# Optimization experiments

Measured on AMD Instinct MI355X. Metric: run time of the kernel, lower is better.

The kernel has to match this reference:

```python
import jax, jax.numpy as jnp
import numpy as np

H = 1024
N_HEADS = 8
HEAD_DIM = H // N_HEADS
META_DIM = 256
VOCAB = 32000
MIN_W, MAX_W = 0.1, 5.0
LN_EPS = 1e-5


def _ln(x, g, b):
    mu = jnp.mean(x, axis=-1, keepdims=True)
    var = jnp.var(x, axis=-1, keepdims=True)
    return (x - mu) * jax.lax.rsqrt(var + LN_EPS) * g + b


def setup_inputs() -> dict:
    key = jax.random.key(0)
    ks = jax.random.split(key, 16)
    B, S = 4, 2048
    s = 0.02
    return {
        "hidden_states": jax.random.normal(ks[0], (B, S, H), jnp.float32),
        "token_ids": jax.random.randint(ks[1], (B, S), 0, VOCAB, jnp.int32),
        "attention_mask": jnp.ones((B, S), jnp.bool_),
        "pos_embed": jax.random.normal(ks[2], (1, S, H), jnp.float32),
        # torch nn.MultiheadAttention params
        "in_proj_w": jax.random.normal(ks[3], (3 * H, H), jnp.float32) * s,
        "in_proj_b": jnp.zeros((3 * H,), jnp.float32),
        "out_w": jax.random.normal(ks[4], (H, H), jnp.float32) * s,
        "out_b": jnp.zeros((H,), jnp.float32),
        # meta_network params (torch Linear convention: y = x @ W.T + b)
        "w1": jax.random.normal(ks[5], (META_DIM, 2 * H), jnp.float32) * s,
        "b1": jnp.zeros((META_DIM,), jnp.float32),
        "g1": jnp.ones((META_DIM,), jnp.float32),
        "beta1": jnp.zeros((META_DIM,), jnp.float32),
        "w2": jax.random.normal(ks[6], (META_DIM // 2, META_DIM), jnp.float32) * s,
        "b2": jnp.zeros((META_DIM // 2,), jnp.float32),
        "g2": jnp.ones((META_DIM // 2,), jnp.float32),
        "beta2": jnp.zeros((META_DIM // 2,), jnp.float32),
        "w3": jax.random.normal(ks[7], (1, META_DIM // 2), jnp.float32) * s,
        "b3": jnp.zeros((1,), jnp.float32),
        # tensorized ImportanceMemory.get_importance: one scalar per vocab id
        "importance_table": jax.random.uniform(ks[8], (VOCAB,), jnp.float32) * 0.1,
    }


def reference(hidden_states, token_ids, attention_mask, pos_embed,
              in_proj_w, in_proj_b, out_w, out_b,
              w1, b1, g1, beta1, w2, b2, g2, beta2, w3, b3,
              importance_table):
    B, S, _ = hidden_states.shape
    x = hidden_states + pos_embed[:, :S, :]

    # MultiheadAttention (batch_first, eval mode -> no dropout)
    qkv = x @ in_proj_w.T + in_proj_b                      # [B,S,3H]
    q, k, v = jnp.split(qkv, 3, axis=-1)
    q = q.reshape(B, S, N_HEADS, HEAD_DIM)
    k = k.reshape(B, S, N_HEADS, HEAD_DIM)
    v = v.reshape(B, S, N_HEADS, HEAD_DIM)
    scores = jnp.einsum('bqhd,bkhd->bhqk', q, k) / jnp.sqrt(jnp.float32(HEAD_DIM))
    scores = jnp.where(attention_mask[:, None, None, :], scores, jnp.float32(-1e9))
    attn = jax.nn.softmax(scores, axis=-1)
    ctx = jnp.einsum('bhqk,bkhd->bqhd', attn, v).reshape(B, S, H)
    attended = ctx @ out_w.T + out_b

    combined = jnp.concatenate([x, attended], axis=-1)     # [B,S,2H]
    h = jax.nn.relu(_ln(combined @ w1.T + b1, g1, beta1))
    h = jax.nn.relu(_ln(h @ w2.T + b2, g2, beta2))
    base_weights = (h @ w3.T + b3).squeeze(-1)             # [B,S]

    # tensorized per-token importance lookup + clamp (manual_weights empty)
    importance = importance_table[token_ids]               # gather [B,S]
    weight = jnp.clip(base_weights * (1.0 + importance), MIN_W, MAX_W)
    return jnp.where(attention_mask, weight, 0.0)
```

## Files before the change

kernel.cpp:

```cpp
#include <hip/hip_runtime.h>
#include <hip/hip_bf16.h>
#include <math.h>

typedef __bf16 bf16;
typedef bf16 bf16x8 __attribute__((ext_vector_type(8)));
typedef bf16 bf16x4 __attribute__((ext_vector_type(4)));
typedef float f32x4 __attribute__((ext_vector_type(4)));

#define HDIM 1024
#define NHEADS 8
#define HD 128
#define MD1 256
#define MD2 128
#define LNEPS 1e-5f

__device__ __forceinline__ f32x4 mfma16(bf16x8 a, bf16x8 b, f32x4 c) {
  return __builtin_amdgcn_mfma_f32_16x16x32_bf16(a, b, c, 0, 0, 0);
}

__device__ __forceinline__ void gload_lds16(const bf16* g, bf16* l) {
  __builtin_amdgcn_global_load_lds(
      (const __attribute__((address_space(1))) void*)g,
      (__attribute__((address_space(3))) void*)l, 16, 0, 0);
}

__global__ void k_prep(const float* __restrict__ hs, const float* __restrict__ pos,
                       bf16* __restrict__ xbf, int SH, int total) {
  int i = (blockIdx.x * blockDim.x + threadIdx.x) * 4;
  if (i >= total) return;
  float4 a = *(const float4*)(hs + i);
  float4 p = *(const float4*)(pos + (i % SH));
  bf16x4 o;
  o[0] = (bf16)(a.x + p.x);
  o[1] = (bf16)(a.y + p.y);
  o[2] = (bf16)(a.z + p.z);
  o[3] = (bf16)(a.w + p.w);
  *(bf16x4*)(xbf + i) = o;
}

__global__ void k_cvt(const float* __restrict__ in, bf16* __restrict__ out, int n) {
  int i = (blockIdx.x * blockDim.x + threadIdx.x) * 4;
  if (i >= n) return;
  float4 v = *(const float4*)(in + i);
  bf16x4 o;
  o[0] = (bf16)v.x; o[1] = (bf16)v.y; o[2] = (bf16)v.z; o[3] = (bf16)v.w;
  *(bf16x4*)(out + i) = o;
}

template<bool OUT_BF>
__global__ __launch_bounds__(256) void k_gemm128(
    const bf16* __restrict__ A, const bf16* __restrict__ Bw,
    const float* __restrict__ bias, void* __restrict__ out,
    int N, int K) {
  __shared__ bf16 As[128 * 32];
  __shared__ bf16 Bs[128 * 32];
  const int tid = threadIdx.x;
  const int w = tid >> 6, lane = tid & 63;
  const int quad = lane >> 4, l16 = lane & 15;
  const int wm = w & 1, wn = w >> 1;
  const int tm = blockIdx.x * 128, tn = blockIdx.y * 128;

  const int r0 = tid >> 2;
  const int f0 = (r0 ^ (r0 >> 2)) & 3;
  const int f1 = ((r0 + 64) ^ ((r0 + 64) >> 2)) & 3;
  const int c0 = (((tid & 3) ^ f0) * 8);
  const int c1 = (((tid & 3) ^ f1) * 8);
  const bf16* a0 = A + (size_t)(tm + r0) * K + c0;
  const bf16* a1 = A + (size_t)(tm + r0 + 64) * K + c1;
  const bf16* b0 = Bw + (size_t)(tn + r0) * K + c0;
  const bf16* b1 = Bw + (size_t)(tn + r0 + 64) * K + c1;
  bf16* lA = As + (size_t)tid * 8;
  bf16* lB = Bs + (size_t)tid * 8;

  f32x4 acc[4][4] = {};
  for (int k0 = 0; k0 < K; k0 += 32) {
    gload_lds16(a0 + k0, lA);
    gload_lds16(a1 + k0, lA + 2048);
    gload_lds16(b0 + k0, lB);
    gload_lds16(b1 + k0, lB + 2048);
    __syncthreads();
    bf16x8 af[4], bfr[4];
#pragma unroll
    for (int mt = 0; mt < 4; ++mt) {
      const int r = wm * 64 + mt * 16 + l16;
      af[mt] = *(const bf16x8*)&As[r * 32 + ((quad ^ ((r ^ (r >> 2)) & 3)) << 3)];
    }
#pragma unroll
    for (int nt = 0; nt < 4; ++nt) {
      const int r = wn * 64 + nt * 16 + l16;
      bfr[nt] = *(const bf16x8*)&Bs[r * 32 + ((quad ^ ((r ^ (r >> 2)) & 3)) << 3)];
    }
#pragma unroll
    for (int mt = 0; mt < 4; ++mt)
#pragma unroll
      for (int nt = 0; nt < 4; ++nt)
        acc[mt][nt] = mfma16(af[mt], bfr[nt], acc[mt][nt]);
    __syncthreads();
  }

#pragma unroll
  for (int nt = 0; nt < 4; ++nt) {
    const int col = tn + wn * 64 + nt * 16 + l16;
    const float bv = bias ? bias[col] : 0.f;
#pragma unroll
    for (int mt = 0; mt < 4; ++mt) {
#pragma unroll
      for (int i = 0; i < 4; ++i) {
        const int row = tm + wm * 64 + mt * 16 + quad * 4 + i;
        const float v = acc[mt][nt][i] + bv;
        if (OUT_BF) ((bf16*)out)[(size_t)row * N + col] = (bf16)v;
        else        ((float*)out)[(size_t)row * N + col] = v;
      }
    }
  }
}

template<bool OUT_BF>
__global__ __launch_bounds__(256) void k_gemm_bt(
    const bf16* __restrict__ A1, const bf16* __restrict__ A2, int K1, int K2,
    const bf16* __restrict__ Bw, const float* __restrict__ bias,
    void* __restrict__ out, int N) {
  const int K = K1 + K2;
  __shared__ bf16 As[64][40];
  __shared__ bf16 Bs[64][40];
  const int tid = threadIdx.x;
  const int w = tid >> 6, lane = tid & 63;
  const int quad = lane >> 4, l16 = lane & 15;
  const int tm = blockIdx.x * 64, tn = blockIdx.y * 64;
  const int lr = tid >> 2;
  const int lc = (tid & 3) * 8;

  f32x4 acc[4] = {};
  for (int k0 = 0; k0 < K; k0 += 32) {
    const int kg = k0 + lc;
    const bf16* ap = (kg < K1) ? (A1 + (size_t)(tm + lr) * K1 + kg)
                               : (A2 + (size_t)(tm + lr) * K2 + (kg - K1));
    *(bf16x8*)&As[lr][lc] = *(const bf16x8*)ap;
    *(bf16x8*)&Bs[lr][lc] = *(const bf16x8*)(Bw + (size_t)(tn + lr) * K + kg);
    __syncthreads();
    bf16x8 af = *(const bf16x8*)&As[w * 16 + l16][quad * 8];
#pragma unroll
    for (int c = 0; c < 4; ++c) {
      bf16x8 bfrag = *(const bf16x8*)&Bs[c * 16 + l16][quad * 8];
      acc[c] = mfma16(af, bfrag, acc[c]);
    }
    __syncthreads();
  }
#pragma unroll
  for (int c = 0; c < 4; ++c) {
    const int col = tn + c * 16 + l16;
    const float bv = bias ? bias[col] : 0.f;
#pragma unroll
    for (int i = 0; i < 4; ++i) {
      const int row = tm + w * 16 + quad * 4 + i;
      const float v = acc[c][i] + bv;
      if (OUT_BF) ((bf16*)out)[(size_t)row * N + col] = (bf16)v;
      else        ((float*)out)[(size_t)row * N + col] = v;
    }
  }
}

__global__ __launch_bounds__(256) void k_flash(
    const bf16* __restrict__ qkv, const int* __restrict__ mask,
    bf16* __restrict__ ctx, int S) {
  __shared__ bf16 Ks[64][136];
  __shared__ bf16 Vt[128 * 64];
  __shared__ bf16 Ps[4 * 16 * 64];
  __shared__ float biass[64];
  const int tid = threadIdx.x, w = tid >> 6, lane = tid & 63;
  const int quad = lane >> 4, l16 = lane & 15;
  const int bh = blockIdx.y, b = bh / NHEADS, h = bh % NHEADS;
  const int q0 = blockIdx.x * 64 + w * 16;
  const size_t rstride = 3 * HDIM;
  const bf16* Qb = qkv + (size_t)b * S * rstride + h * HD;
  const bf16* Kb = Qb + HDIM;
  const bf16* Vb = Qb + 2 * HDIM;
  const int* mrow = mask + (size_t)b * S;

  bf16x8 qf[4];
#pragma unroll
  for (int s = 0; s < 4; ++s)
    qf[s] = *(const bf16x8*)(Qb + (size_t)(q0 + l16) * rstride + s * 32 + quad * 8);

  float lsum[4] = {0.f, 0.f, 0.f, 0.f};
  f32x4 o[8] = {};
  const float scale2 = 0.08838834764831845f * 1.4426950408889634f;

  const int nchunk = S / 64;
  bf16x8 kreg[4], vreg[4];
  int mreg = (tid < 64) ? mrow[tid] : 0;
#pragma unroll
  for (int it = 0; it < 4; ++it) {
    const int cid = tid + it * 256, row = cid >> 4, d8 = (cid & 15) * 8;
    kreg[it] = *(const bf16x8*)(Kb + (size_t)row * rstride + d8);
    vreg[it] = *(const bf16x8*)(Vb + (size_t)row * rstride + d8);
  }

  for (int c0 = 0; c0 < nchunk; ++c0) {
    __syncthreads();
#pragma unroll
    for (int it = 0; it < 4; ++it) {
      const int cid = tid + it * 256, row = cid >> 4, d8 = (cid & 15) * 8;
      *(bf16x8*)&Ks[row][d8] = kreg[it];
      const int rb = row >> 3, rlo = row & 7;
#pragma unroll
      for (int j = 0; j < 8; ++j) {
        const int d = d8 + j;
        const int blk = rb ^ ((d ^ (d >> 3)) & 7);
        Vt[d * 64 + blk * 8 + rlo] = vreg[it][j];
      }
    }
    if (tid < 64) biass[tid] = mreg ? 0.f : -1e9f;
    __syncthreads();
    const int cn = (c0 + 1 < nchunk) ? c0 + 1 : c0;
    const int key0n = cn * 64;
    if (tid < 64) mreg = mrow[key0n + tid];
#pragma unroll
    for (int it = 0; it < 4; ++it) {
      const int cid = tid + it * 256, row = cid >> 4, d8 = (cid & 15) * 8;
      kreg[it] = *(const bf16x8*)(Kb + (size_t)(key0n + row) * rstride + d8);
      vreg[it] = *(const bf16x8*)(Vb + (size_t)(key0n + row) * rstride + d8);
    }
#pragma unroll
    for (int g = 0; g < 4; ++g) {
      f32x4 s4 = {};
#pragma unroll
      for (int s = 0; s < 4; ++s) {
        bf16x8 kf = *(const bf16x8*)&Ks[g * 16 + l16][s * 32 + quad * 8];
        s4 = mfma16(qf[s], kf, s4);
      }
      const float bias = biass[g * 16 + l16];
      const int kb2 = 2 * g + (l16 >> 3), klo = l16 & 7;
#pragma unroll
      for (int i = 0; i < 4; ++i) {
        const float p = exp2f(fmaf(s4[i], scale2, bias));
        lsum[i] += p;
        const int r = quad * 4 + i;
        Ps[w * 1024 + r * 64 + ((kb2 ^ (r & 7)) << 3) + klo] = (bf16)p;
      }
    }
#pragma unroll
    for (int hh = 0; hh < 2; ++hh) {
      bf16x8 pf = *(const bf16x8*)&Ps[w * 1024 + l16 * 64 + (((hh * 4 + quad) ^ (l16 & 7)) << 3)];
#pragma unroll
      for (int dg = 0; dg < 8; ++dg) {
        const int d = dg * 16 + l16;
        const int blk = (hh * 4 + quad) ^ ((d ^ (d >> 3)) & 7);
        bf16x8 vf = *(const bf16x8*)&Vt[d * 64 + blk * 8];
        o[dg] = mfma16(pf, vf, o[dg]);
      }
    }
  }

#pragma unroll
  for (int i = 0; i < 4; ++i) {
#pragma unroll
    for (int off = 1; off < 16; off <<= 1) lsum[i] += __shfl_xor(lsum[i], off);
    const int row = q0 + quad * 4 + i;
    const float inv = 1.0f / lsum[i];
#pragma unroll
    for (int dg = 0; dg < 8; ++dg)
      ctx[((size_t)b * S + row) * HDIM + h * HD + dg * 16 + l16] = (bf16)(o[dg][i] * inv);
  }
}

__global__ __launch_bounds__(256) void k_ln1(const float* __restrict__ y,
                                             const float* __restrict__ g,
                                             const float* __restrict__ be,
                                             bf16* __restrict__ out) {
  const int w = threadIdx.x >> 6, lane = threadIdx.x & 63;
  const int row = blockIdx.x * 4 + w;
  const float* yr = y + (size_t)row * MD1;
  float4 v = *(const float4*)(yr + lane * 4);
  float s = v.x + v.y + v.z + v.w;
  float q = v.x * v.x + v.y * v.y + v.z * v.z + v.w * v.w;
#pragma unroll
  for (int off = 1; off < 64; off <<= 1) { s += __shfl_xor(s, off); q += __shfl_xor(q, off); }
  const float mean = s / MD1;
  const float var = q / MD1 - mean * mean;
  const float r = rsqrtf(var + LNEPS);
  bf16* orow = out + (size_t)row * MD1;
  const float xv[4] = {v.x, v.y, v.z, v.w};
#pragma unroll
  for (int j = 0; j < 4; ++j) {
    const int c = lane * 4 + j;
    float t = (xv[j] - mean) * r * g[c] + be[c];
    orow[c] = (bf16)fmaxf(t, 0.f);
  }
}

__global__ __launch_bounds__(256) void k_final(
    const float* __restrict__ y2, const float* __restrict__ g2,
    const float* __restrict__ be2, const float* __restrict__ w3,
    const float* __restrict__ b3, const int* __restrict__ tok,
    const int* __restrict__ msk, const float* __restrict__ imp,
    float* __restrict__ out) {
  const int w = threadIdx.x >> 6, lane = threadIdx.x & 63;
  const int row = blockIdx.x * 4 + w;
  const float* yr = y2 + (size_t)row * MD2;
  const float2 v = *(const float2*)(yr + lane * 2);
  float s = v.x + v.y, q = v.x * v.x + v.y * v.y;
#pragma unroll
  for (int off = 1; off < 64; off <<= 1) { s += __shfl_xor(s, off); q += __shfl_xor(q, off); }
  const float mean = s / MD2;
  const float var = q / MD2 - mean * mean;
  const float r = rsqrtf(var + LNEPS);
  float acc = 0.f;
  const float xv[2] = {v.x, v.y};
#pragma unroll
  for (int j = 0; j < 2; ++j) {
    const int c = lane * 2 + j;
    float t = (xv[j] - mean) * r * g2[c] + be2[c];
    acc += fmaxf(t, 0.f) * w3[c];
  }
#pragma unroll
  for (int off = 1; off < 64; off <<= 1) acc += __shfl_xor(acc, off);
  if (lane == 0) {
    const float base = acc + b3[0];
    float wt = base * (1.f + imp[tok[row]]);
    wt = fminf(fmaxf(wt, 0.1f), 5.0f);
    out[row] = msk[row] ? wt : 0.f;
  }
}

extern "C" void kernel_launch(void* const* d_in, const int* in_sizes, int n_in,
                              void* d_out, int out_size, void* d_ws, size_t ws_size,
                              hipStream_t stream) {
  const float* hs  = (const float*)d_in[0];
  const int*   tok = (const int*)d_in[1];
  const int*   msk = (const int*)d_in[2];
  const float* pos = (const float*)d_in[3];
  const float* inw = (const float*)d_in[4];
  const float* inb = (const float*)d_in[5];
  const float* ow  = (const float*)d_in[6];
  const float* ob  = (const float*)d_in[7];
  const float* w1  = (const float*)d_in[8];
  const float* b1  = (const float*)d_in[9];
  const float* g1  = (const float*)d_in[10];
  const float* be1 = (const float*)d_in[11];
  const float* w2  = (const float*)d_in[12];
  const float* b2  = (const float*)d_in[13];
  const float* g2  = (const float*)d_in[14];
  const float* be2 = (const float*)d_in[15];
  const float* w3  = (const float*)d_in[16];
  const float* b3  = (const float*)d_in[17];
  const float* imp = (const float*)d_in[18];

  const int SH = in_sizes[3];
  const int S  = SH / HDIM;
  const int Bsz = in_sizes[0] / SH;
  const int M = Bsz * S;

  char* ws = (char*)d_ws;
  size_t off = 0;
  bf16* xbf = (bf16*)(ws + off);        off += (size_t)M * HDIM * 2;
  bf16* qkvbf = (bf16*)(ws + off);
  bf16* attbf = qkvbf;
  float* y1 = (float*)(ws + off + (size_t)M * HDIM * 2);
  bf16* h1 = (bf16*)((char*)y1 + (size_t)M * MD1 * 4);
  float* y2 = (float*)((char*)h1 + (size_t)M * MD1 * 2);
  off += (size_t)M * 3 * HDIM * 2;
  bf16* ctx = (bf16*)(ws + off);        off += (size_t)M * HDIM * 2;
  bf16* winp = (bf16*)(ws + off);       off += (size_t)3 * HDIM * HDIM * 2;
  bf16* wout = (bf16*)(ws + off);       off += (size_t)HDIM * HDIM * 2;
  bf16* w1b = (bf16*)(ws + off);        off += (size_t)MD1 * 2 * HDIM * 2;
  bf16* w2b = (bf16*)(ws + off);        off += (size_t)MD2 * MD1 * 2;

  {
    int total = M * HDIM;
    k_prep<<<total / 4 / 256, 256, 0, stream>>>(hs, pos, xbf, SH, total);
  }
  k_cvt<<<(3 * HDIM * HDIM) / 4 / 256, 256, 0, stream>>>(inw, winp, 3 * HDIM * HDIM);
  k_cvt<<<(HDIM * HDIM) / 4 / 256, 256, 0, stream>>>(ow, wout, HDIM * HDIM);
  k_cvt<<<(MD1 * 2 * HDIM) / 4 / 256, 256, 0, stream>>>(w1, w1b, MD1 * 2 * HDIM);
  k_cvt<<<(MD2 * MD1) / 4 / 256, 256, 0, stream>>>(w2, w2b, MD2 * MD1);
  k_gemm128<true><<<dim3(M / 128, (3 * HDIM) / 128), 256, 0, stream>>>(
      xbf, winp, inb, qkvbf, 3 * HDIM, HDIM);
  k_flash<<<dim3(S / 64, Bsz * NHEADS), 256, 0, stream>>>(qkvbf, msk, ctx, S);
  k_gemm128<true><<<dim3(M / 128, HDIM / 128), 256, 0, stream>>>(
      ctx, wout, ob, attbf, HDIM, HDIM);
  k_gemm_bt<false><<<dim3(M / 64, MD1 / 64), 256, 0, stream>>>(
      xbf, attbf, HDIM, HDIM, w1b, b1, y1, MD1);
  k_ln1<<<M / 4, 256, 0, stream>>>(y1, g1, be1, h1);
  k_gemm_bt<false><<<dim3(M / 64, MD2 / 64), 256, 0, stream>>>(
      h1, h1, MD1, 0, w2b, b2, y2, MD2);
  k_final<<<M / 4, 256, 0, stream>>>(y2, g2, be2, w3, b3, tok, msk, imp,
                                     (float*)d_out);
}
```

Baseline: 423.3 us.

## Split QKV into separate Q/K/transposed-V buffers and widen flash tile to 128 queries

```diff
diff --git a/kernel.cpp b/kernel.cpp
--- a/kernel.cpp
+++ b/kernel.cpp
@@ -38,13 +38,20 @@
   *(bf16x4*)(xbf + i) = o;
 }
 
-__global__ void k_cvt(const float* __restrict__ in, bf16* __restrict__ out, int n) {
+__global__ void k_cvt4(const float* __restrict__ s0, bf16* __restrict__ d0, int n0,
+                       const float* __restrict__ s1, bf16* __restrict__ d1, int n1,
+                       const float* __restrict__ s2, bf16* __restrict__ d2, int n2,
+                       const float* __restrict__ s3, bf16* __restrict__ d3, int n3) {
   int i = (blockIdx.x * blockDim.x + threadIdx.x) * 4;
-  if (i >= n) return;
-  float4 v = *(const float4*)(in + i);
+  const float* s; bf16* d;
+  if (i < n0)                { s = s0 + i; d = d0 + i; }
+  else if (i < n0 + n1)      { s = s1 + (i - n0); d = d1 + (i - n0); }
+  else if (i < n0 + n1 + n2) { s = s2 + (i - n0 - n1); d = d2 + (i - n0 - n1); }
+  else                       { s = s3 + (i - n0 - n1 - n2); d = d3 + (i - n0 - n1 - n2); }
+  float4 v = *(const float4*)s;
   bf16x4 o;
   o[0] = (bf16)v.x; o[1] = (bf16)v.y; o[2] = (bf16)v.z; o[3] = (bf16)v.w;
-  *(bf16x4*)(out + i) = o;
+  *(bf16x4*)d = o;
 }
 
 template<bool OUT_BF>
@@ -113,6 +120,198 @@
       }
     }
   }
+}
+
+__global__ __launch_bounds__(256) void k_gemm_qkv(
+    const bf16* __restrict__ A, const bf16* __restrict__ Bw,
+    const float* __restrict__ bias, bf16* __restrict__ Qo,
+    bf16* __restrict__ Ko, bf16* __restrict__ VTo, int S, int K) {
+  __shared__ bf16 As[128 * 32];
+  __shared__ bf16 Bs[128 * 32];
+  const int tid = threadIdx.x;
+  const int w = tid >> 6, lane = tid & 63;
+  const int quad = lane >> 4, l16 = lane & 15;
+  const int wm = w & 1, wn = w >> 1;
+  const int tm = blockIdx.x * 128, tn = blockIdx.y * 128;
+
+  const int r0 = tid >> 2;
+  const int f0 = (r0 ^ (r0 >> 2)) & 3;
+  const int f1 = ((r0 + 64) ^ ((r0 + 64) >> 2)) & 3;
+  const int c0 = (((tid & 3) ^ f0) * 8);
+  const int c1 = (((tid & 3) ^ f1) * 8);
+  const bf16* a0 = A + (size_t)(tm + r0) * K + c0;
+  const bf16* a1 = A + (size_t)(tm + r0 + 64) * K + c1;
+  const bf16* b0 = Bw + (size_t)(tn + r0) * K + c0;
+  const bf16* b1 = Bw + (size_t)(tn + r0 + 64) * K + c1;
+  bf16* lA = As + (size_t)tid * 8;
+  bf16* lB = Bs + (size_t)tid * 8;
+
+  f32x4 acc[4][4] = {};
+  for (int k0 = 0; k0 < K; k0 += 32) {
+    gload_lds16(a0 + k0, lA);
+    gload_lds16(a1 + k0, lA + 2048);
+    gload_lds16(b0 + k0, lB);
+    gload_lds16(b1 + k0, lB + 2048);
+    __syncthreads();
+    bf16x8 af[4], bfr[4];
+#pragma unroll
+    for (int mt = 0; mt < 4; ++mt) {
+      const int r = wm * 64 + mt * 16 + l16;
+      af[mt] = *(const bf16x8*)&As[r * 32 + ((quad ^ ((r ^ (r >> 2)) & 3)) << 3)];
+    }
+#pragma unroll
+    for (int nt = 0; nt < 4; ++nt) {
+      const int r = wn * 64 + nt * 16 + l16;
+      bfr[nt] = *(const bf16x8*)&Bs[r * 32 + ((quad ^ ((r ^ (r >> 2)) & 3)) << 3)];
+    }
+#pragma unroll
+    for (int mt = 0; mt < 4; ++mt)
+#pragma unroll
+      for (int nt = 0; nt < 4; ++nt)
+        acc[mt][nt] = mfma16(af[mt], bfr[nt], acc[mt][nt]);
+    __syncthreads();
+  }
+
+  const int region = tn >> 10;
+  const int btile = tm / S, s0 = tm % S;
+#pragma unroll
+  for (int nt = 0; nt < 4; ++nt) {
+    const int col = tn + wn * 64 + nt * 16 + l16;
+    const float bv = bias[col];
+#pragma unroll
+    for (int mt = 0; mt < 4; ++mt) {
+      if (region == 2) {
+        const int d = col - 2048, hh = d >> 7, dd = d & 127;
+        const int sb = s0 + wm * 64 + mt * 16 + quad * 4;
+        bf16x4 o4;
+#pragma unroll
+        for (int i = 0; i < 4; ++i) o4[i] = (bf16)(acc[mt][nt][i] + bv);
+        *(bf16x4*)&VTo[((size_t)(btile * NHEADS + hh) * HD + dd) * S + sb] = o4;
+      } else {
+        bf16* dst = (region == 0) ? Qo : Ko;
+        const int cc = (region == 0) ? col : col - 1024;
+#pragma unroll
+        for (int i = 0; i < 4; ++i) {
+          const int row = tm + wm * 64 + mt * 16 + quad * 4 + i;
+          dst[(size_t)row * HDIM + cc] = (bf16)(acc[mt][nt][i] + bv);
+        }
+      }
+    }
+  }
+}
+
+__global__ __launch_bounds__(256) void k_flash(
+    const bf16* __restrict__ Qg, const bf16* __restrict__ Kg,
+    const bf16* __restrict__ VTg, const int* __restrict__ mask,
+    bf16* __restrict__ ctx, int S) {
+  __shared__ bf16 Ks[64][136];
+  __shared__ bf16 Vt[128 * 64];
+  __shared__ bf16 Ps[8 * 1024];
+  __shared__ float biass[64];
+  const int tid = threadIdx.x, w = tid >> 6, lane = tid & 63;
+  const int quad = lane >> 4, l16 = lane & 15;
+  const int bh = blockIdx.y, b = bh / NHEADS, h = bh % NHEADS;
+  const int q0 = blockIdx.x * 128 + w * 32;
+  const size_t bS = (size_t)b * S;
+  const bf16* Qb = Qg + bS * HDIM + h * HD;
+  const bf16* Kb = Kg + bS * HDIM + h * HD;
+  const bf16* Vb = VTg + (size_t)bh * HD * S;
+  const int* mrow = mask + bS;
+
+  bf16x8 qf[2][4];
+#pragma unroll
+  for (int qt = 0; qt < 2; ++qt)
+#pragma unroll
+    for (int s = 0; s < 4; ++s)
+      qf[qt][s] = *(const bf16x8*)(Qb + (size_t)(q0 + qt * 16 + l16) * HDIM + s * 32 + quad * 8);
+
+  float lsum[2][4] = {};
+  f32x4 o[2][8] = {};
+  const float scale2 = 0.08838834764831845f * 1.4426950408889634f;
+
+  const int nchunk = S / 64;
+  bf16x8 kreg[4], vreg[4];
+  int mreg = (tid < 64) ? mrow[tid] : 0;
+#pragma unroll
+  for (int it = 0; it < 4; ++it) {
+    const int cid = tid + it * 256;
+    kreg[it] = *(const bf16x8*)(Kb + (size_t)(cid >> 4) * HDIM + (cid & 15) * 8);
+    vreg[it] = *(const bf16x8*)(Vb + (size_t)(cid >> 3) * S + (cid & 7) * 8);
+  }
+
+  for (int c0 = 0; c0 < nchunk; ++c0) {
+    __syncthreads();
+#pragma unroll
+    for (int it = 0; it < 4; ++it) {
+      const int cid = tid + it * 256;
+      *(bf16x8*)&Ks[cid >> 4][(cid & 15) * 8] = kreg[it];
+      const int vd = cid >> 3, vkb = cid & 7;
+      *(bf16x8*)&Vt[vd * 64 + ((vkb ^ (vd & 7)) << 3)] = vreg[it];
+    }
+    if (tid < 64) biass[tid] = mreg ? 0.f : -1e9f;
+    __syncthreads();
+    const int key0n = ((c0 + 1 < nchunk) ? c0 + 1 : c0) * 64;
+    if (tid < 64) mreg = mrow[key0n + tid];
+#pragma unroll
+    for (int it = 0; it < 4; ++it) {
+      const int cid = tid + it * 256;
+      kreg[it] = *(const bf16x8*)(Kb + (size_t)(key0n + (cid >> 4)) * HDIM + (cid & 15) * 8);
+      vreg[it] = *(const bf16x8*)(Vb + (size_t)(cid >> 3) * S + key0n + (cid & 7) * 8);
+    }
+    f32x4 s4[2][4] = {};
+#pragma unroll
+    for (int g = 0; g < 4; ++g)
+#pragma unroll
+      for (int s = 0; s < 4; ++s) {
+        bf16x8 kf = *(const bf16x8*)&Ks[g * 16 + l16][s * 32 + quad * 8];
+        s4[0][g] = mfma16(qf[0][s], kf, s4[0][g]);
+        s4[1][g] = mfma16(qf[1][s], kf, s4[1][g]);
+      }
+#pragma unroll
+    for (int qt = 0; qt < 2; ++qt) {
+      const int base = (w * 2 + qt) * 1024;
+#pragma unroll
+      for (int g = 0; g < 4; ++g) {
+        const float bias = biass[g * 16 + l16];
+        const int kb2 = 2 * g + (l16 >> 3), klo = l16 & 7;
+#pragma unroll
+        for (int i = 0; i < 4; ++i) {
+          const float p = exp2f(fmaf(s4[qt][g][i], scale2, bias));
+          lsum[qt][i] += p;
+          const int r = quad * 4 + i, fr = (r ^ (r >> 3)) & 7;
+          Ps[base + r * 64 + ((kb2 ^ fr) << 3) + klo] = (bf16)p;
+        }
+      }
+    }
+    const int fl = (l16 ^ (l16 >> 3)) & 7;
+#pragma unroll
+    for (int hh = 0; hh < 2; ++hh) {
+      const int kb = hh * 4 + quad;
+      bf16x8 pf0 = *(const bf16x8*)&Ps[(w * 2) * 1024 + l16 * 64 + ((kb ^ fl) << 3)];
+      bf16x8 pf1 = *(const bf16x8*)&Ps[(w * 2 + 1) * 1024 + l16 * 64 + ((kb ^ fl) << 3)];
+#pragma unroll
+      for (int dg = 0; dg < 8; ++dg) {
+        const int d = dg * 16 + l16;
+        bf16x8 vf = *(const bf16x8*)&Vt[d * 64 + ((kb ^ (d & 7)) << 3)];
+        o[0][dg] = mfma16(pf0, vf, o[0][dg]);
+        o[1][dg] = mfma16(pf1, vf, o[1][dg]);
+      }
+    }
+  }
+
+#pragma unroll
+  for (int qt = 0; qt < 2; ++qt)
+#pragma unroll
+    for (int i = 0; i < 4; ++i) {
+      float ls = lsum[qt][i];
+#pragma unroll
+      for (int off = 1; off < 16; off <<= 1) ls += __shfl_xor(ls, off);
+      const int row = q0 + qt * 16 + quad * 4 + i;
+      const float inv = 1.0f / ls;
+#pragma unroll
+      for (int dg = 0; dg < 8; ++dg)
+        ctx[(bS + row) * HDIM + h * HD + dg * 16 + l16] = (bf16)(o[qt][dg][i] * inv);
+    }
 }
 
 template<bool OUT_BF>
@@ -157,110 +356,6 @@
       if (OUT_BF) ((bf16*)out)[(size_t)row * N + col] = (bf16)v;
       else        ((float*)out)[(size_t)row * N + col] = v;
     }
-  }
-}
-
-__global__ __launch_bounds__(256) void k_flash(
-    const bf16* __restrict__ qkv, const int* __restrict__ mask,
-    bf16* __restrict__ ctx, int S) {
-  __shared__ bf16 Ks[64][136];
-  __shared__ bf16 Vt[128 * 64];
-  __shared__ bf16 Ps[4 * 16 * 64];
-  __shared__ float biass[64];
-  const int tid = threadIdx.x, w = tid >> 6, lane = tid & 63;
-  const int quad = lane >> 4, l16 = lane & 15;
-  const int bh = blockIdx.y, b = bh / NHEADS, h = bh % NHEADS;
-  const int q0 = blockIdx.x * 64 + w * 16;
-  const size_t rstride = 3 * HDIM;
-  const bf16* Qb = qkv + (size_t)b * S * rstride + h * HD;
-  const bf16* Kb = Qb + HDIM;
-  const bf16* Vb = Qb + 2 * HDIM;
-  const int* mrow = mask + (size_t)b * S;
-
-  bf16x8 qf[4];
-#pragma unroll
-  for (int s = 0; s < 4; ++s)
-    qf[s] = *(const bf16x8*)(Qb + (size_t)(q0 + l16) * rstride + s * 32 + quad * 8);
-
-  float lsum[4] = {0.f, 0.f, 0.f, 0.f};
-  f32x4 o[8] = {};
-  const float scale2 = 0.08838834764831845f * 1.4426950408889634f;
-
-  const int nchunk = S / 64;
-  bf16x8 kreg[4], vreg[4];
-  int mreg = (tid < 64) ? mrow[tid] : 0;
-#pragma unroll
-  for (int it = 0; it < 4; ++it) {
-    const int cid = tid + it * 256, row = cid >> 4, d8 = (cid & 15) * 8;
-    kreg[it] = *(const bf16x8*)(Kb + (size_t)row * rstride + d8);
-    vreg[it] = *(const bf16x8*)(Vb + (size_t)row * rstride + d8);
-  }
-
-  for (int c0 = 0; c0 < nchunk; ++c0) {
-    __syncthreads();
-#pragma unroll
-    for (int it = 0; it < 4; ++it) {
-      const int cid = tid + it * 256, row = cid >> 4, d8 = (cid & 15) * 8;
-      *(bf16x8*)&Ks[row][d8] = kreg[it];
-      const int rb = row >> 3, rlo = row & 7;
-#pragma unroll
-      for (int j = 0; j < 8; ++j) {
-        const int d = d8 + j;
-        const int blk = rb ^ ((d ^ (d >> 3)) & 7);
-        Vt[d * 64 + blk * 8 + rlo] = vreg[it][j];
-      }
-    }
-    if (tid < 64) biass[tid] = mreg ? 0.f : -1e9f;
-    __syncthreads();
-    const int cn = (c0 + 1 < nchunk) ? c0 + 1 : c0;
-    const int key0n = cn * 64;
-    if (tid < 64) mreg = mrow[key0n + tid];
-#pragma unroll
-    for (int it = 0; it < 4; ++it) {
-      const int cid = tid + it * 256, row = cid >> 4, d8 = (cid & 15) * 8;
-      kreg[it] = *(const bf16x8*)(Kb + (size_t)(key0n + row) * rstride + d8);
-      vreg[it] = *(const bf16x8*)(Vb + (size_t)(key0n + row) * rstride + d8);
-    }
-#pragma unroll
-    for (int g = 0; g < 4; ++g) {
-      f32x4 s4 = {};
-#pragma unroll
-      for (int s = 0; s < 4; ++s) {
-        bf16x8 kf = *(const bf16x8*)&Ks[g * 16 + l16][s * 32 + quad * 8];
-        s4 = mfma16(qf[s], kf, s4);
-      }
-      const float bias = biass[g * 16 + l16];
-      const int kb2 = 2 * g + (l16 >> 3), klo = l16 & 7;
-#pragma unroll
-      for (int i = 0; i < 4; ++i) {
-        const float p = exp2f(fmaf(s4[i], scale2, bias));
-        lsum[i] += p;
-        const int r = quad * 4 + i;
-        Ps[w * 1024 + r * 64 + ((kb2 ^ (r & 7)) << 3) + klo] = (bf16)p;
-      }
-    }
-#pragma unroll
-    for (int hh = 0; hh < 2; ++hh) {
-      bf16x8 pf = *(const bf16x8*)&Ps[w * 1024 + l16 * 64 + (((hh * 4 + quad) ^ (l16 & 7)) << 3)];
-#pragma unroll
-      for (int dg = 0; dg < 8; ++dg) {
-        const int d = dg * 16 + l16;
-        const int blk = (hh * 4 + quad) ^ ((d ^ (d >> 3)) & 7);
-        bf16x8 vf = *(const bf16x8*)&Vt[d * 64 + blk * 8];
-        o[dg] = mfma16(pf, vf, o[dg]);
-      }
-    }
-  }
-
-#pragma unroll
-  for (int i = 0; i < 4; ++i) {
-#pragma unroll
-    for (int off = 1; off < 16; off <<= 1) lsum[i] += __shfl_xor(lsum[i], off);
-    const int row = q0 + quad * 4 + i;
-    const float inv = 1.0f / lsum[i];
-#pragma unroll
-    for (int dg = 0; dg < 8; ++dg)
-      ctx[((size_t)b * S + row) * HDIM + h * HD + dg * 16 + l16] = (bf16)(o[dg][i] * inv);
   }
 }
 
@@ -352,31 +447,34 @@
   const int M = Bsz * S;
 
   char* ws = (char*)d_ws;
+  const size_t MB2 = (size_t)M * HDIM * 2;
   size_t off = 0;
-  bf16* xbf = (bf16*)(ws + off);        off += (size_t)M * HDIM * 2;
-  bf16* qkvbf = (bf16*)(ws + off);
-  bf16* attbf = qkvbf;
-  float* y1 = (float*)(ws + off + (size_t)M * HDIM * 2);
-  bf16* h1 = (bf16*)((char*)y1 + (size_t)M * MD1 * 4);
-  float* y2 = (float*)((char*)h1 + (size_t)M * MD1 * 2);
-  off += (size_t)M * 3 * HDIM * 2;
-  bf16* ctx = (bf16*)(ws + off);        off += (size_t)M * HDIM * 2;
-  bf16* winp = (bf16*)(ws + off);       off += (size_t)3 * HDIM * HDIM * 2;
-  bf16* wout = (bf16*)(ws + off);       off += (size_t)HDIM * HDIM * 2;
-  bf16* w1b = (bf16*)(ws + off);        off += (size_t)MD1 * 2 * HDIM * 2;
-  bf16* w2b = (bf16*)(ws + off);        off += (size_t)MD2 * MD1 * 2;
+  bf16* xbf = (bf16*)(ws + off);  off += MB2;
+  bf16* Qb  = (bf16*)(ws + off);  off += MB2;
+  bf16* Kb  = (bf16*)(ws + off);  off += MB2;
+  bf16* VTb = (bf16*)(ws + off);  off += MB2;
+  bf16* ctx = (bf16*)(ws + off);  off += MB2;
+  bf16* winp = (bf16*)(ws + off); off += (size_t)3 * HDIM * HDIM * 2;
+  bf16* wout = (bf16*)(ws + off); off += (size_t)HDIM * HDIM * 2;
+  bf16* w1b = (bf16*)(ws + off);  off += (size_t)MD1 * 2 * HDIM * 2;
+  bf16* w2b = (bf16*)(ws + off);  off += (size_t)MD2 * MD1 * 2;
+  bf16* attbf = Qb;
+  float* y1 = (float*)Kb;
+  bf16*  h1 = VTb;
+  float* y2 = (float*)ctx;
 
   {
     int total = M * HDIM;
     k_prep<<<total / 4 / 256, 256, 0, stream>>>(hs, pos, xbf, SH, total);
   }
-  k_cvt<<<(3 * HDIM * HDIM) / 4 / 256, 256, 0, stream>>>(inw, winp, 3 * HDIM * HDIM);
-  k_cvt<<<(HDIM * HDIM) / 4 / 256, 256, 0, stream>>>(ow, wout, HDIM * HDIM);
-  k_cvt<<<(MD1 * 2 * HDIM) / 4 / 256, 256, 0, stream>>>(w1, w1b, MD1 * 2 * HDIM);
-  k_cvt<<<(MD2 * MD1) / 4 / 256, 256, 0, stream>>>(w2, w2b, MD2 * MD1);
-  k_gemm128<true><<<dim3(M / 128, (3 * HDIM) / 128), 256, 0, stream>>>(
-      xbf, winp, inb, qkvbf, 3 * HDIM, HDIM);
-  k_flash<<<dim3(S / 64, Bsz * NHEADS), 256, 0, stream>>>(qkvbf, msk, ctx, S);
+  {
+    const int n0 = 3 * HDIM * HDIM, n1 = HDIM * HDIM, n2 = MD1 * 2 * HDIM, n3 = MD2 * MD1;
+    k_cvt4<<<(n0 + n1 + n2 + n3) / 4 / 256, 256, 0, stream>>>(
+        inw, winp, n0, ow, wout, n1, w1, w1b, n2, w2, w2b, n3);
+  }
+  k_gemm_qkv<<<dim3(M / 128, (3 * HDIM) / 128), 256, 0, stream>>>(
+      xbf, winp, inb, Qb, Kb, VTb, S, HDIM);
+  k_flash<<<dim3(S / 128, Bsz * NHEADS), 256, 0, stream>>>(Qb, Kb, VTb, msk, ctx, S);
   k_gemm128<true><<<dim3(M / 128, HDIM / 128), 256, 0, stream>>>(
       ctx, wout, ob, attbf, HDIM, HDIM);
   k_gemm_bt<false><<<dim3(M / 64, MD1 / 64), 256, 0, stream>>>(
```

New measurement: 414.3 us. 2.1% less time.
